# Kernel tuning notes

Measured on AMD Instinct MI355X. Metric: run time of the kernel, lower is better.

Reference implementation:

```python
import jax, jax.numpy as jnp
import numpy as np
import math

D_MODEL = 1024
NUM_HEADS = 16
HEAD_DIM = D_MODEL // NUM_HEADS
BATCH = 2
SEQ = 2048
NEG_INF = -1000000.0  # matches torch code's -1e6 fill


def setup_inputs() -> dict:
    key = jax.random.key(0)
    ks = jax.random.split(key, 10)
    s = 1.0 / math.sqrt(D_MODEL)
    inp = {
        "X": jax.random.normal(ks[0], (BATCH, SEQ, D_MODEL), dtype=jnp.float32),
        "Wq": jax.random.uniform(ks[1], (D_MODEL, D_MODEL), minval=-s, maxval=s, dtype=jnp.float32),
        "bq": jnp.zeros((D_MODEL,), jnp.float32),
        "Wk": jax.random.uniform(ks[2], (D_MODEL, D_MODEL), minval=-s, maxval=s, dtype=jnp.float32),
        "bk": jnp.zeros((D_MODEL,), jnp.float32),
        "Wv": jax.random.uniform(ks[3], (D_MODEL, D_MODEL), minval=-s, maxval=s, dtype=jnp.float32),
        "bv": jnp.zeros((D_MODEL,), jnp.float32),
        "Wo": jax.random.uniform(ks[4], (D_MODEL, D_MODEL), minval=-s, maxval=s, dtype=jnp.float32),
        "bo": jnp.zeros((D_MODEL,), jnp.float32),
        "valid_lens": jax.random.randint(ks[5], (BATCH, NUM_HEADS), 1, SEQ + 1, dtype=jnp.int64)
        if jax.config.jax_enable_x64 else
        jax.random.randint(ks[5], (BATCH, NUM_HEADS), 1, SEQ + 1, dtype=jnp.int32),
    }
    return inp


def _split_heads(Y, B, S):
    # (B, S, D) -> (B*H, S, head_dim), matching transpose_qkv
    return Y.reshape(B, S, NUM_HEADS, HEAD_DIM).transpose(0, 2, 1, 3).reshape(B * NUM_HEADS, S, HEAD_DIM)


def reference(X, Wq, bq, Wk, bk, Wv, bv, Wo, bo, valid_lens):
    B, S, D = X.shape
    q = _split_heads(X @ Wq.T + bq, B, S)
    k = _split_heads(X @ Wk.T + bk, B, S)
    v = _split_heads(X @ Wv.T + bv, B, S)
    scores = jnp.einsum("bqd,bkd->bqk", q, k) / math.sqrt(HEAD_DIM)  # (B*H, S, S)
    # Faithful to torch code: 2-D valid_lens reshaped to (B*H,), mask over
    # the first two dims -> entire query rows j >= valid_len set to -1e6.
    row_mask = jnp.arange(S)[None, :] < valid_lens.reshape(-1)[:, None]  # (B*H, S)
    scores = jnp.where(row_mask[:, :, None], scores, NEG_INF)
    attn = jax.nn.softmax(scores, axis=-1)
    out = jnp.einsum("bqk,bkd->bqd", attn, v)  # (B*H, S, head_dim)
    out = out.reshape(B, NUM_HEADS, S, HEAD_DIM).transpose(0, 2, 1, 3).reshape(B, S, D)
    return out @ Wo.T + bo
```

## Files before the change

### kernel.cpp

```cpp
#include <hip/hip_runtime.h>

#define SQ 2048
#define DM 1024
#define NH 16
#define HD 64

typedef __bf16 bf16x8 __attribute__((ext_vector_type(8)));
typedef float f32x4 __attribute__((ext_vector_type(4)));
typedef unsigned short u16;
typedef unsigned int u32;

__device__ __forceinline__ u16 f2b(float f) {
  union { float f; u32 u; } c; c.f = f;
  return (u16)((c.u + 0x7FFFu + ((c.u >> 16) & 1u)) >> 16);
}

__device__ __forceinline__ void gll16(const void* g, void* l) {
  __builtin_amdgcn_global_load_lds(
      (const __attribute__((address_space(1))) void*)g,
      (__attribute__((address_space(3))) void*)l, 16, 0, 0);
}

__global__ void __launch_bounds__(256) conv_bf16(
    const float* __restrict__ X,
    const float* __restrict__ Wq, const float* __restrict__ Wk,
    const float* __restrict__ Wv, const float* __restrict__ Wo,
    u16* __restrict__ Xb, u16* __restrict__ Wqb, u16* __restrict__ Wkb,
    u16* __restrict__ Wvb, u16* __restrict__ Wob) {
  const size_t e = ((size_t)blockIdx.x * 256 + threadIdx.x) * 8;
  const float* src; u16* dst; size_t rel;
  if (e < 4194304u)      { src = X;  dst = Xb;  rel = e; }
  else if (e < 5242880u) { src = Wq; dst = Wqb; rel = e - 4194304u; }
  else if (e < 6291456u) { src = Wk; dst = Wkb; rel = e - 5242880u; }
  else if (e < 7340032u) { src = Wv; dst = Wvb; rel = e - 6291456u; }
  else                   { src = Wo; dst = Wob; rel = e - 7340032u; }
  float4 a = *(const float4*)(src + rel);
  float4 b = *(const float4*)(src + rel + 4);
  union { u16 h[8]; uint4 v; } o;
  o.h[0] = f2b(a.x); o.h[1] = f2b(a.y); o.h[2] = f2b(a.z); o.h[3] = f2b(a.w);
  o.h[4] = f2b(b.x); o.h[5] = f2b(b.y); o.h[6] = f2b(b.z); o.h[7] = f2b(b.w);
  *(uint4*)(dst + rel) = o.v;
}

__device__ __forceinline__ void stage128(const u16* __restrict__ A, const u16* __restrict__ B,
                                         u16* sA, u16* sB, int m0, int n0, int kt,
                                         int w, int l) {
#pragma unroll
  for (int c = 0; c < 2; ++c) {
    const int g = w * 2 + c;
    const int s = g * 64 + l;
    const int r = s >> 2, cc = s & 3;
    gll16(A + (size_t)(m0 + r) * DM + kt * 32 + cc * 8, sA + g * 512);
    gll16(B + (size_t)(n0 + r) * DM + kt * 32 + cc * 8, sB + g * 512);
  }
}

__device__ __forceinline__ void gemm_core2(const u16* __restrict__ A, const u16* __restrict__ B,
                                           u16* sA, u16* sB,
                                           int m0, int n0, f32x4 acc[4][4]) {
  const int t = threadIdx.x, l = t & 63, w = t >> 6;
  const int wr = w >> 1, wc = w & 1, lg = l >> 4, li = l & 15;

  stage128(A, B, sA, sB, m0, n0, 0, w, l);
  __syncthreads();
  int cur = 0;
  for (int kt = 0; kt < DM / 32; ++kt) {
    if (kt + 1 < DM / 32)
      stage128(A, B, sA + (cur ^ 1) * 4096, sB + (cur ^ 1) * 4096, m0, n0, kt + 1, w, l);
    bf16x8 aF[4], bF[4];
#pragma unroll
    for (int mi = 0; mi < 4; ++mi)
      aF[mi] = *(const bf16x8*)(sA + cur * 4096 + (wr * 64 + mi * 16 + li) * 32 + lg * 8);
#pragma unroll
    for (int ni = 0; ni < 4; ++ni)
      bF[ni] = *(const bf16x8*)(sB + cur * 4096 + (wc * 64 + ni * 16 + li) * 32 + lg * 8);
#pragma unroll
    for (int mi = 0; mi < 4; ++mi)
#pragma unroll
      for (int ni = 0; ni < 4; ++ni)
        acc[mi][ni] = __builtin_amdgcn_mfma_f32_16x16x32_bf16(aF[mi], bF[ni], acc[mi][ni], 0, 0, 0);
    __syncthreads();
    cur ^= 1;
  }
}

__global__ void __launch_bounds__(256) qkv_gemm(
    const u16* __restrict__ Xb, const u16* __restrict__ Wqkv,
    const float* __restrict__ bq, const float* __restrict__ bk, const float* __restrict__ bv,
    u16* __restrict__ Qb, u16* __restrict__ Kb, u16* __restrict__ Vt) {
  __shared__ u16 sA[8192];
  __shared__ u16 sB[8192];
  const int m0 = blockIdx.y * 128, n0 = blockIdx.x * 128;
  const int mode = n0 >> 10;
  const float* bias = (mode == 0) ? bq : (mode == 1) ? bk : bv;

  f32x4 acc[4][4];
  f32x4 z4 = {0.f, 0.f, 0.f, 0.f};
#pragma unroll
  for (int i = 0; i < 4; ++i)
#pragma unroll
    for (int j = 0; j < 4; ++j) acc[i][j] = z4;

  gemm_core2(Xb, Wqkv, sA, sB, m0, n0, acc);

  const int t = threadIdx.x;
  const int l = t & 63, w = t >> 6;
  const int wr = w >> 1, wc = w & 1, lg = l >> 4, li = l & 15;
#pragma unroll
  for (int mi = 0; mi < 4; ++mi) {
    const int m = m0 + wr * 64 + mi * 16 + lg * 4;
    const int b = m >> 11;
    const int s = m & 2047;
#pragma unroll
    for (int ni = 0; ni < 4; ++ni) {
      const int n = n0 + wc * 64 + ni * 16 + li;
      const int nn = n - (mode << 10);
      const int h = nn >> 6, dd = nn & 63;
      const float bia = bias[nn];
      const size_t bh = (size_t)(b * NH + h);
      if (mode == 2) {
        union { u16 h4[4]; uint2 u; } pk;
#pragma unroll
        for (int r = 0; r < 4; ++r) pk.h4[r] = f2b(acc[mi][ni][r] + bia);
        *(uint2*)(Vt + (bh * HD + dd) * SQ + s) = pk.u;
      } else {
#pragma unroll
        for (int r = 0; r < 4; ++r) {
          const float val = acc[mi][ni][r] + bia;
          const int ss = s + r;
          if (mode == 0) Qb[(bh * SQ + ss) * HD + dd] = f2b(val * 0.180336880f);
          else           Kb[(bh * SQ + ss) * HD + dd] = f2b(val);
        }
      }
    }
  }
}

__global__ void __launch_bounds__(256) out_gemm(
    const u16* __restrict__ Ag, const u16* __restrict__ Wob,
    const float* __restrict__ bo, float* __restrict__ out) {
  __shared__ u16 sA[2][2048];
  __shared__ u16 sB[2][4096];
  const int t = threadIdx.x, l = t & 63, w = t >> 6;
  const int wr = w >> 1, wc = w & 1, lg = l >> 4, li = l & 15;
  const int m0 = blockIdx.y * 64, n0 = blockIdx.x * 128;

  auto stage = [&](int buf, int kt) {
    {
      const int s = w * 64 + l;
      const int r = s >> 2, cc = s & 3;
      gll16(Ag + (size_t)(m0 + r) * DM + kt * 32 + cc * 8, &sA[buf][w * 512]);
    }
#pragma unroll
    for (int c = 0; c < 2; ++c) {
      const int g = w * 2 + c;
      const int s = g * 64 + l;
      const int r = s >> 2, cc = s & 3;
      gll16(Wob + (size_t)(n0 + r) * DM + kt * 32 + cc * 8, &sB[buf][g * 512]);
    }
  };

  f32x4 acc[2][4];
  f32x4 z4 = {0.f, 0.f, 0.f, 0.f};
#pragma unroll
  for (int i = 0; i < 2; ++i)
#pragma unroll
    for (int j = 0; j < 4; ++j) acc[i][j] = z4;

  stage(0, 0);
  __syncthreads();
  int cur = 0;
  for (int kt = 0; kt < DM / 32; ++kt) {
    if (kt + 1 < DM / 32) stage(cur ^ 1, kt + 1);
    bf16x8 aF[2], bF[4];
#pragma unroll
    for (int mi = 0; mi < 2; ++mi)
      aF[mi] = *(const bf16x8*)(&sA[cur][(wr * 32 + mi * 16 + li) * 32 + lg * 8]);
#pragma unroll
    for (int ni = 0; ni < 4; ++ni)
      bF[ni] = *(const bf16x8*)(&sB[cur][(wc * 64 + ni * 16 + li) * 32 + lg * 8]);
#pragma unroll
    for (int mi = 0; mi < 2; ++mi)
#pragma unroll
      for (int ni = 0; ni < 4; ++ni)
        acc[mi][ni] = __builtin_amdgcn_mfma_f32_16x16x32_bf16(aF[mi], bF[ni], acc[mi][ni], 0, 0, 0);
    __syncthreads();
    cur ^= 1;
  }

#pragma unroll
  for (int mi = 0; mi < 2; ++mi) {
    const int m = m0 + wr * 32 + mi * 16 + lg * 4;
#pragma unroll
    for (int ni = 0; ni < 4; ++ni) {
      const int n = n0 + wc * 64 + ni * 16 + li;
      const float bia = bo[n];
#pragma unroll
      for (int r = 0; r < 4; ++r)
        out[(size_t)(m + r) * DM + n] = acc[mi][ni][r] + bia;
    }
  }
}

__global__ void __launch_bounds__(256) attn_v9(
    const u16* __restrict__ Qb, const u16* __restrict__ Kb, const u16* __restrict__ Vt,
    const int* __restrict__ vlen, u16* __restrict__ Ao) {
  __shared__ u16 sK[2][4096];
  __shared__ u16 sV[2][4096];
  const int bh = blockIdx.x, qt = blockIdx.y;
  const int t = threadIdx.x, w = t >> 6, l = t & 63, lg = l >> 4, li = l & 15;
  const int vl = vlen[bh];
  const u16* Qh = Qb + (size_t)bh * SQ * HD;
  const u16* Kh = Kb + (size_t)bh * SQ * HD;
  const u16* Vh = Vt + (size_t)bh * HD * SQ;
  const int q0 = qt * 64 + w * 16;

  const bool mq = (q0 + li) >= vl;
  bf16x8 qf[2];
#pragma unroll
  for (int kk = 0; kk < 2; ++kk) {
    qf[kk] = *(const bf16x8*)(Qh + (size_t)(q0 + li) * HD + kk * 32 + lg * 8);
    if (mq) {
      union { u32 u[4]; bf16x8 v; } z; z.u[0] = z.u[1] = z.u[2] = z.u[3] = 0;
      qf[kk] = z.v;
    }
  }

  union { u16 h[8]; bf16x8 v; } onesU;
#pragma unroll
  for (int j = 0; j < 8; ++j) onesU.h[j] = 0x3F80;
  const bf16x8 ones = onesU.v;

  int gq[2]; int kOff[2], vOff[2];
#pragma unroll
  for (int c = 0; c < 2; ++c) {
    gq[c] = w * 2 + c;
    const int s = gq[c] * 64 + l;
    const int r = s >> 3, cs = s & 7;
    const int csrc = cs ^ (r & 7);
    const int sig = (r & 32) | (((r >> 2) & 3) << 3) | (((r >> 4) & 1) << 2) | (r & 3);
    kOff[c] = sig * HD + csrc * 8;
    vOff[c] = r * SQ + csrc * 8;
  }
  auto stageKV = [&](int buf, int kt) {
#pragma unroll
    for (int c = 0; c < 2; ++c) {
      gll16(Kh + (size_t)(kt * 64) * HD + kOff[c], &sK[buf][gq[c] * 512]);
      gll16(Vh + (size_t)(kt * 64) + vOff[c], &sV[buf][gq[c] * 512]);
    }
  };

  f32x4 z4 = {0.f, 0.f, 0.f, 0.f};
  f32x4 acc[4], lacc;
#pragma unroll
  for (int ni = 0; ni < 4; ++ni) acc[ni] = z4;
  lacc = z4;

  stageKV(0, 0);
  __syncthreads();
  int cur = 0;
  for (int kt = 0; kt < SQ / 64; ++kt) {
    if (kt + 1 < SQ / 64) stageKV(cur ^ 1, kt + 1);

    f32x4 sc[4];
#pragma unroll
    for (int ni = 0; ni < 4; ++ni) {
      const int row = ni * 16 + li;
      bf16x8 kf0 = *(const bf16x8*)(&sK[cur][row * 64 + ((lg ^ (row & 7)) * 8)]);
      bf16x8 kf1 = *(const bf16x8*)(&sK[cur][row * 64 + (((4 + lg) ^ (row & 7)) * 8)]);
      sc[ni] = __builtin_amdgcn_mfma_f32_16x16x32_bf16(kf0, qf[0], z4, 0, 0, 0);
      sc[ni] = __builtin_amdgcn_mfma_f32_16x16x32_bf16(kf1, qf[1], sc[ni], 0, 0, 0);
    }

    bf16x8 pb[2];
#pragma unroll
    for (int h = 0; h < 2; ++h) {
      union { __bf16 e[8]; bf16x8 v; } P;
#pragma unroll
      for (int j = 0; j < 4; ++j) {
        P.e[j]     = (__bf16)__builtin_amdgcn_exp2f(sc[2 * h][j]);
        P.e[4 + j] = (__bf16)__builtin_amdgcn_exp2f(sc[2 * h + 1][j]);
      }
      pb[h] = P.v;
    }

    lacc = __builtin_amdgcn_mfma_f32_16x16x32_bf16(ones, pb[0], lacc, 0, 0, 0);
    lacc = __builtin_amdgcn_mfma_f32_16x16x32_bf16(ones, pb[1], lacc, 0, 0, 0);

#pragma unroll
    for (int ni = 0; ni < 4; ++ni) {
      const int row = ni * 16 + li;
      bf16x8 vf0 = *(const bf16x8*)(&sV[cur][row * 64 + ((lg ^ (row & 7)) * 8)]);
      bf16x8 vf1 = *(const bf16x8*)(&sV[cur][row * 64 + (((4 + lg) ^ (row & 7)) * 8)]);
      acc[ni] = __builtin_amdgcn_mfma_f32_16x16x32_bf16(vf0, pb[0], acc[ni], 0, 0, 0);
      acc[ni] = __builtin_amdgcn_mfma_f32_16x16x32_bf16(vf1, pb[1], acc[ni], 0, 0, 0);
    }

    __syncthreads();
    cur ^= 1;
  }

  const int b = bh >> 4, h = bh & 15;
  const float inv = 1.0f / lacc[0];
  const size_t rowb = ((size_t)(b * SQ + q0 + li)) * DM + h * HD;
#pragma unroll
  for (int ni = 0; ni < 4; ++ni) {
    union { __bf16 h2[4]; uint2 u; } ov;
#pragma unroll
    for (int r = 0; r < 4; ++r) ov.h2[r] = (__bf16)(acc[ni][r] * inv);
    *(uint2*)(Ao + rowb + ni * 16 + lg * 4) = ov.u;
  }
}

extern "C" void kernel_launch(void* const* d_in, const int* in_sizes, int n_in,
                              void* d_out, int out_size, void* d_ws, size_t ws_size,
                              hipStream_t stream) {
  const float* X  = (const float*)d_in[0];
  const float* Wq = (const float*)d_in[1];
  const float* bq = (const float*)d_in[2];
  const float* Wk = (const float*)d_in[3];
  const float* bk = (const float*)d_in[4];
  const float* Wv = (const float*)d_in[5];
  const float* bv = (const float*)d_in[6];
  const float* Wo = (const float*)d_in[7];
  const float* bo = (const float*)d_in[8];
  const int* vlen = (const int*)d_in[9];

  char* ws = (char*)d_ws;
  u16* Qb  = (u16*)(ws);
  u16* Kb  = (u16*)(ws + (size_t)8388608);
  u16* Vt  = (u16*)(ws + (size_t)16777216);
  u16* Xb  = (u16*)(ws + (size_t)25165824);
  u16* Ao  = Xb;
  u16* Wqb = (u16*)(ws + (size_t)33554432);
  u16* Wkb = (u16*)(ws + (size_t)35651584);
  u16* Wvb = (u16*)(ws + (size_t)37748736);
  u16* Wob = (u16*)(ws + (size_t)39845888);

  dim3 blk(256);
  conv_bf16<<<4096, blk, 0, stream>>>(X, Wq, Wk, Wv, Wo, Xb, Wqb, Wkb, Wvb, Wob);
  qkv_gemm<<<dim3(24, 32), blk, 0, stream>>>(Xb, Wqb, bq, bk, bv, Qb, Kb, Vt);
  attn_v9<<<dim3(32, 32), blk, 0, stream>>>(Qb, Kb, Vt, vlen, Ao);
  out_gemm<<<dim3(8, 64), blk, 0, stream>>>(Ao, Wob, bo, (float*)d_out);
}
```

Baseline: 122.9 us.

## Split attention key range across warps with per-warp LDS pipelines and cross-warp reduction

Each warp now covers all 64 query rows of the block but only a 512-key slice, instead of 16 query rows over all keys. Each warp stages its own K/V tiles into a private double buffer with explicit vmcnt waits, which removes the per-iteration block-wide barriers. At the end, partial outputs and row sums are reduced through LDS. The change trades much higher register use (16 accumulators plus 8 Q fragments) and a final reduction pass for less synchronisation and for reusing the K/V fragments across four query groups.

```diff
diff --git a/kernel.cpp b/kernel.cpp
--- a/kernel.cpp
+++ b/kernel.cpp
@@ -202,27 +202,31 @@
   }
 }
 
-__global__ void __launch_bounds__(256) attn_v9(
+__global__ void __launch_bounds__(256, 2) attn_v10(
     const u16* __restrict__ Qb, const u16* __restrict__ Kb, const u16* __restrict__ Vt,
     const int* __restrict__ vlen, u16* __restrict__ Ao) {
-  __shared__ u16 sK[2][4096];
-  __shared__ u16 sV[2][4096];
+  __shared__ u16 sKV[4][2][4096];
+  __shared__ float lpart[4][4][16];
   const int bh = blockIdx.x, qt = blockIdx.y;
   const int t = threadIdx.x, w = t >> 6, l = t & 63, lg = l >> 4, li = l & 15;
   const int vl = vlen[bh];
   const u16* Qh = Qb + (size_t)bh * SQ * HD;
   const u16* Kh = Kb + (size_t)bh * SQ * HD;
   const u16* Vh = Vt + (size_t)bh * HD * SQ;
-  const int q0 = qt * 64 + w * 16;
-
-  const bool mq = (q0 + li) >= vl;
-  bf16x8 qf[2];
-#pragma unroll
-  for (int kk = 0; kk < 2; ++kk) {
-    qf[kk] = *(const bf16x8*)(Qh + (size_t)(q0 + li) * HD + kk * 32 + lg * 8);
-    if (mq) {
-      union { u32 u[4]; bf16x8 v; } z; z.u[0] = z.u[1] = z.u[2] = z.u[3] = 0;
-      qf[kk] = z.v;
+  const int q0 = qt * 64;
+  const int k0 = w * 512;
+
+  bf16x8 qf[4][2];
+#pragma unroll
+  for (int g = 0; g < 4; ++g) {
+    const bool mq = (q0 + g * 16 + li) >= vl;
+#pragma unroll
+    for (int kk = 0; kk < 2; ++kk) {
+      qf[g][kk] = *(const bf16x8*)(Qh + (size_t)(q0 + g * 16 + li) * HD + kk * 32 + lg * 8);
+      if (mq) {
+        union { u32 u[4]; bf16x8 v; } z; z.u[0] = z.u[1] = z.u[2] = z.u[3] = 0;
+        qf[g][kk] = z.v;
+      }
     }
   }
 
@@ -231,84 +235,115 @@
   for (int j = 0; j < 8; ++j) onesU.h[j] = 0x3F80;
   const bf16x8 ones = onesU.v;
 
-  int gq[2]; int kOff[2], vOff[2];
-#pragma unroll
-  for (int c = 0; c < 2; ++c) {
-    gq[c] = w * 2 + c;
-    const int s = gq[c] * 64 + l;
-    const int r = s >> 3, cs = s & 7;
-    const int csrc = cs ^ (r & 7);
-    const int sig = (r & 32) | (((r >> 2) & 3) << 3) | (((r >> 4) & 1) << 2) | (r & 3);
-    kOff[c] = sig * HD + csrc * 8;
-    vOff[c] = r * SQ + csrc * 8;
-  }
-  auto stageKV = [&](int buf, int kt) {
-#pragma unroll
-    for (int c = 0; c < 2; ++c) {
-      gll16(Kh + (size_t)(kt * 64) * HD + kOff[c], &sK[buf][gq[c] * 512]);
-      gll16(Vh + (size_t)(kt * 64) + vOff[c], &sV[buf][gq[c] * 512]);
-    }
+  int kOff[4], vOff[4];
+#pragma unroll
+  for (int i = 0; i < 4; ++i) {
+    {
+      const int s = i * 64 + l, row = s >> 3, c = s & 7;
+      const int csrc = c ^ (row & 7);
+      const int sig = (((row >> 2) & 3) << 3) | (((row >> 4) & 1) << 2) | (row & 3);
+      kOff[i] = sig * HD + csrc * 8;
+    }
+    {
+      const int s = i * 64 + l, d = s >> 2, c = s & 3;
+      const int csrc = c ^ (d & 3);
+      vOff[i] = d * SQ + csrc * 8;
+    }
+  }
+
+  u16* sw = &sKV[w][0][0];
+  auto stage = [&](int buf, int tt) {
+    const u16* kb = Kh + (size_t)(k0 + tt * 32) * HD;
+    const u16* vb = Vh + (size_t)(k0 + tt * 32);
+    u16* db = sw + buf * 4096;
+#pragma unroll
+    for (int i = 0; i < 4; ++i) gll16(kb + kOff[i], db + i * 512);
+#pragma unroll
+    for (int i = 0; i < 4; ++i) gll16(vb + vOff[i], db + 2048 + i * 512);
   };
 
   f32x4 z4 = {0.f, 0.f, 0.f, 0.f};
-  f32x4 acc[4], lacc;
-#pragma unroll
-  for (int ni = 0; ni < 4; ++ni) acc[ni] = z4;
-  lacc = z4;
-
-  stageKV(0, 0);
+  f32x4 acc[4][4], lacc[4];
+#pragma unroll
+  for (int g = 0; g < 4; ++g) {
+    lacc[g] = z4;
+#pragma unroll
+    for (int n2 = 0; n2 < 4; ++n2) acc[g][n2] = z4;
+  }
+
+  stage(0, 0);
+  int cur = 0;
+  for (int tt = 0; tt < 16; ++tt) {
+    if (tt < 15) {
+      stage(cur ^ 1, tt + 1);
+      asm volatile("s_waitcnt vmcnt(8)" ::: "memory");
+    } else {
+      asm volatile("s_waitcnt vmcnt(0)" ::: "memory");
+    }
+    const u16* kb_ = sw + cur * 4096;
+    const u16* vb_ = sw + cur * 4096 + 2048;
+
+    bf16x8 kf[2][2], vf[4];
+#pragma unroll
+    for (int ni = 0; ni < 2; ++ni) {
+      const int row = ni * 16 + li;
+      kf[ni][0] = *(const bf16x8*)(kb_ + row * 64 + ((lg ^ (row & 7)) * 8));
+      kf[ni][1] = *(const bf16x8*)(kb_ + row * 64 + (((4 + lg) ^ (row & 7)) * 8));
+    }
+#pragma unroll
+    for (int n2 = 0; n2 < 4; ++n2) {
+      const int d = n2 * 16 + li;
+      vf[n2] = *(const bf16x8*)(vb_ + d * 32 + ((lg ^ (d & 3)) * 8));
+    }
+
+#pragma unroll
+    for (int g = 0; g < 4; ++g) {
+      f32x4 s0 = __builtin_amdgcn_mfma_f32_16x16x32_bf16(kf[0][0], qf[g][0], z4, 0, 0, 0);
+      s0 = __builtin_amdgcn_mfma_f32_16x16x32_bf16(kf[0][1], qf[g][1], s0, 0, 0, 0);
+      f32x4 s1 = __builtin_amdgcn_mfma_f32_16x16x32_bf16(kf[1][0], qf[g][0], z4, 0, 0, 0);
+      s1 = __builtin_amdgcn_mfma_f32_16x16x32_bf16(kf[1][1], qf[g][1], s1, 0, 0, 0);
+
+      union { __bf16 e[8]; bf16x8 v; } P;
+#pragma unroll
+      for (int r = 0; r < 4; ++r) {
+        P.e[r]     = (__bf16)__builtin_amdgcn_exp2f(s0[r]);
+        P.e[4 + r] = (__bf16)__builtin_amdgcn_exp2f(s1[r]);
+      }
+
+      lacc[g] = __builtin_amdgcn_mfma_f32_16x16x32_bf16(ones, P.v, lacc[g], 0, 0, 0);
+#pragma unroll
+      for (int n2 = 0; n2 < 4; ++n2)
+        acc[g][n2] = __builtin_amdgcn_mfma_f32_16x16x32_bf16(vf[n2], P.v, acc[g][n2], 0, 0, 0);
+    }
+    cur ^= 1;
+  }
+
   __syncthreads();
-  int cur = 0;
-  for (int kt = 0; kt < SQ / 64; ++kt) {
-    if (kt + 1 < SQ / 64) stageKV(cur ^ 1, kt + 1);
-
-    f32x4 sc[4];
-#pragma unroll
-    for (int ni = 0; ni < 4; ++ni) {
-      const int row = ni * 16 + li;
-      bf16x8 kf0 = *(const bf16x8*)(&sK[cur][row * 64 + ((lg ^ (row & 7)) * 8)]);
-      bf16x8 kf1 = *(const bf16x8*)(&sK[cur][row * 64 + (((4 + lg) ^ (row & 7)) * 8)]);
-      sc[ni] = __builtin_amdgcn_mfma_f32_16x16x32_bf16(kf0, qf[0], z4, 0, 0, 0);
-      sc[ni] = __builtin_amdgcn_mfma_f32_16x16x32_bf16(kf1, qf[1], sc[ni], 0, 0, 0);
-    }
-
-    bf16x8 pb[2];
-#pragma unroll
-    for (int h = 0; h < 2; ++h) {
-      union { __bf16 e[8]; bf16x8 v; } P;
-#pragma unroll
-      for (int j = 0; j < 4; ++j) {
-        P.e[j]     = (__bf16)__builtin_amdgcn_exp2f(sc[2 * h][j]);
-        P.e[4 + j] = (__bf16)__builtin_amdgcn_exp2f(sc[2 * h + 1][j]);
-      }
-      pb[h] = P.v;
-    }
-
-    lacc = __builtin_amdgcn_mfma_f32_16x16x32_bf16(ones, pb[0], lacc, 0, 0, 0);
-    lacc = __builtin_amdgcn_mfma_f32_16x16x32_bf16(ones, pb[1], lacc, 0, 0, 0);
-
-#pragma unroll
-    for (int ni = 0; ni < 4; ++ni) {
-      const int row = ni * 16 + li;
-      bf16x8 vf0 = *(const bf16x8*)(&sV[cur][row * 64 + ((lg ^ (row & 7)) * 8)]);
-      bf16x8 vf1 = *(const bf16x8*)(&sV[cur][row * 64 + (((4 + lg) ^ (row & 7)) * 8)]);
-      acc[ni] = __builtin_amdgcn_mfma_f32_16x16x32_bf16(vf0, pb[0], acc[ni], 0, 0, 0);
-      acc[ni] = __builtin_amdgcn_mfma_f32_16x16x32_bf16(vf1, pb[1], acc[ni], 0, 0, 0);
-    }
-
-    __syncthreads();
-    cur ^= 1;
-  }
-
+  f32x4* op = (f32x4*)&sKV[0][0][0];
+#pragma unroll
+  for (int g = 0; g < 4; ++g) {
+#pragma unroll
+    for (int n2 = 0; n2 < 4; ++n2)
+      op[(((w * 4) + g) * 4 + n2) * 64 + l] = acc[g][n2];
+    if (lg == 0) lpart[w][g][li] = lacc[g][0];
+  }
+  __syncthreads();
+
+  const int g = w;
+  const float lf = lpart[0][g][li] + lpart[1][g][li] + lpart[2][g][li] + lpart[3][g][li];
+  const float inv = 1.0f / lf;
   const int b = bh >> 4, h = bh & 15;
-  const float inv = 1.0f / lacc[0];
-  const size_t rowb = ((size_t)(b * SQ + q0 + li)) * DM + h * HD;
-#pragma unroll
-  for (int ni = 0; ni < 4; ++ni) {
+  const size_t rowb = ((size_t)(b * SQ + q0 + g * 16 + li)) * DM + h * HD;
+#pragma unroll
+  for (int n2 = 0; n2 < 4; ++n2) {
+    f32x4 s = op[((0 * 4 + g) * 4 + n2) * 64 + l];
+    s += op[((1 * 4 + g) * 4 + n2) * 64 + l];
+    s += op[((2 * 4 + g) * 4 + n2) * 64 + l];
+    s += op[((3 * 4 + g) * 4 + n2) * 64 + l];
     union { __bf16 h2[4]; uint2 u; } ov;
 #pragma unroll
-    for (int r = 0; r < 4; ++r) ov.h2[r] = (__bf16)(acc[ni][r] * inv);
-    *(uint2*)(Ao + rowb + ni * 16 + lg * 4) = ov.u;
+    for (int r = 0; r < 4; ++r) ov.h2[r] = (__bf16)(s[r] * inv);
+    *(uint2*)(Ao + rowb + n2 * 16 + lg * 4) = ov.u;
   }
 }
 
@@ -340,6 +375,6 @@
   dim3 blk(256);
   conv_bf16<<<4096, blk, 0, stream>>>(X, Wq, Wk, Wv, Wo, Xb, Wqb, Wkb, Wvb, Wob);
   qkv_gemm<<<dim3(24, 32), blk, 0, stream>>>(Xb, Wqb, bq, bk, bv, Qb, Kb, Vt);
-  attn_v9<<<dim3(32, 32), blk, 0, stream>>>(Qb, Kb, Vt, vlen, Ao);
+  attn_v10<<<dim3(32, 32), blk, 0, stream>>>(Qb, Kb, Vt, vlen, Ao);
   out_gemm<<<dim3(8, 64), blk, 0, stream>>>(Ao, Wob, bo, (float*)d_out);
 }
```

Result: faster. 119.1 us (-3.1%).
